# Optimization experiments

Measured on AMD Instinct MI355X. Metric: run time of the kernel, lower is better.

The kernel has to match this reference:

```python
import jax, jax.numpy as jnp
import numpy as np

B, N_PER, F = 8, 4096, 64
RATIO, RADIUS, K = 0.25, 0.2, 64
S = int(N_PER * RATIO)  # 1024 samples per cloud
NEG = -1e30


def setup_inputs() -> dict:
    key = jax.random.key(0)
    ks = jax.random.split(key, 8)
    pos = jax.random.uniform(ks[0], (B * N_PER, 3), dtype=jnp.float32)
    x = jax.random.normal(ks[1], (B * N_PER, F), dtype=jnp.float32)
    batch = jnp.repeat(jnp.arange(B, dtype=jnp.int32), N_PER)
    W1 = jax.random.normal(ks[2], (F + 3, 128), dtype=jnp.float32) * 0.05
    b1 = jnp.zeros((128,), jnp.float32)
    W2 = jax.random.normal(ks[3], (128, 128), dtype=jnp.float32) * 0.05
    b2 = jnp.zeros((128,), jnp.float32)
    W3 = jax.random.normal(ks[4], (128, 256), dtype=jnp.float32) * 0.05
    b3 = jnp.zeros((256,), jnp.float32)
    return {"x": x, "pos": pos, "batch": batch,
            "W1": W1, "b1": b1, "W2": W2, "b2": b2, "W3": W3, "b3": b3}


def _fps_single(p):
    """Farthest point sampling on one cloud p:[N,3] -> S int32 indices (seed idx 0)."""
    d0 = jnp.sum((p - p[0]) ** 2, axis=-1)  # [N]

    def step(min_d, _):
        nxt = jnp.argmax(min_d).astype(jnp.int32)
        d = jnp.sum((p - p[nxt]) ** 2, axis=-1)
        return jnp.minimum(min_d, d), nxt

    _, rest = jax.lax.scan(step, d0, None, length=S - 1)
    return jnp.concatenate([jnp.zeros((1,), jnp.int32), rest])


def reference(x, pos, batch, W1, b1, W2, b2, W3, b3):
    pos_b = pos.reshape(B, N_PER, 3)
    x_b = x.reshape(B, N_PER, F)
    batch_b = batch.reshape(B, N_PER)

    # --- FPS sampling (sequential scan, vmapped over clouds) ---
    idx = jax.vmap(_fps_single)(pos_b)                                  # [B,S]
    pos_s = jnp.take_along_axis(pos_b, idx[..., None], axis=1)          # [B,S,3]

    # --- radius neighbor search: nearest K within RADIUS (deterministic) ---
    d2 = jnp.sum((pos_s[:, :, None, :] - pos_b[:, None, :, :]) ** 2, -1)  # [B,S,N]
    neg = jnp.where(d2 <= RADIUS ** 2, -d2, NEG)
    vals, nbr = jax.lax.top_k(neg, K)                                   # [B,S,K]
    valid = vals > NEG / 2                                              # [B,S,K]

    # --- gather neighbor features / positions ---
    x_j = jnp.take_along_axis(x_b[:, None], nbr[..., None], axis=2)     # [B,S,K,F]
    pos_j = jnp.take_along_axis(pos_b[:, None], nbr[..., None], axis=2) # [B,S,K,3]
    rel = pos_j - pos_s[:, :, None, :]                                  # [B,S,K,3]

    # --- edge MLP (Lin+ReLU per PyG PointNetConv local_nn) ---
    h = jnp.concatenate([x_j, rel], axis=-1)                            # [B,S,K,F+3]
    h = jax.nn.relu(h @ W1 + b1)
    h = jax.nn.relu(h @ W2 + b2)
    h = jax.nn.relu(h @ W3 + b3)                                        # [B,S,K,256]

    # --- scatter-max aggregation over neighbors ---
    h = jnp.where(valid[..., None], h, NEG)
    out = jnp.max(h, axis=2)                                            # [B,S,256]
    out = jnp.where(out > NEG / 2, out, 0.0)

    x1 = out.reshape(B * S, -1)
    pos1 = pos_s.reshape(B * S, 3)
    batch1 = jnp.take_along_axis(batch_b, idx, axis=1).reshape(-1)
    return x1, pos1, batch1
```

## Files before the change

### kernel.cpp

```cpp
#include <hip/hip_runtime.h>
#include <hip/hip_bf16.h>
#include <stdint.h>

#define NPER 4096
#define NCLOUD 8
#define FD 64
#define SS 1024
#define NBK 64
#define CAP 512

typedef unsigned int u32;
typedef unsigned long long u64;
typedef __attribute__((ext_vector_type(8))) short short8v;
typedef __attribute__((ext_vector_type(8))) unsigned short ushort8v;
typedef __attribute__((ext_vector_type(4))) float f32x4;

__device__ __forceinline__ float fadd(float a, float b){ return __fadd_rn(a,b); }
__device__ __forceinline__ float fsub(float a, float b){ return __fsub_rn(a,b); }
__device__ __forceinline__ float fmul(float a, float b){ return __fmul_rn(a,b); }
__device__ __forceinline__ float dist2(float ax,float ay,float az,float bx,float by,float bz){
  float dx=fsub(ax,bx), dy=fsub(ay,by), dz=fsub(az,bz);
  return fadd(fadd(fmul(dx,dx),fmul(dy,dy)),fmul(dz,dz));
}
__device__ __forceinline__ unsigned short f2b(float v){
  __hip_bfloat16 h = __float2bfloat16(v);
  return *reinterpret_cast<unsigned short*>(&h);
}

template<int CTRL, int RMASK>
__device__ __forceinline__ float dppmaxf(float v){
  int t = __builtin_amdgcn_update_dpp(0, __float_as_int(v), CTRL, RMASK, 0xf, false);
  return fmaxf(v, __int_as_float(t));
}
template<int CTRL, int RMASK>
__device__ __forceinline__ void kmin_stage(u32& hi, u32& lo){
  u32 hio = (u32)__builtin_amdgcn_update_dpp(-1, (int)hi, CTRL, RMASK, 0xf, false);
  u32 loo = (u32)__builtin_amdgcn_update_dpp(-1, (int)lo, CTRL, RMASK, 0xf, false);
  u64 ko = ((u64)hio<<32)|loo, k = ((u64)hi<<32)|lo;
  bool g = ko < k;
  hi = g?hio:hi; lo = g?loo:lo;
}

#define LOADG(q, j0, j1, j2, j3) { \
    const float4* pv = (const float4*)(pb + (size_t)(base + q*4)*3); \
    float4 v0=pv[0], v1=pv[1], v2=pv[2]; \
    x##j0=v0.x; y##j0=v0.y; z##j0=v0.z; \
    x##j1=v0.w; y##j1=v1.x; z##j1=v1.y; \
    x##j2=v1.z; y##j2=v1.w; z##j2=v2.x; \
    x##j3=v2.y; y##j3=v2.z; z##j3=v2.w; \
    float4 c0; c0.x=x##j0; c0.y=y##j0; c0.z=z##j0; c0.w=0.f; spt[base+q*4+0]=c0; \
    float4 c1; c1.x=x##j1; c1.y=y##j1; c1.z=z##j1; c1.w=0.f; spt[base+q*4+1]=c1; \
    float4 c2; c2.x=x##j2; c2.y=y##j2; c2.z=z##j2; c2.w=0.f; spt[base+q*4+2]=c2; \
    float4 c3; c3.x=x##j3; c3.y=y##j3; c3.z=z##j3; c3.w=0.f; spt[base+q*4+3]=c3; \
  }
#define DINIT(j) m##j = dist2(x##j,y##j,z##j,p0x,p0y,p0z);
#define DUPD(j)  { float d = dist2(x##j,y##j,z##j,pnx,pny,pnz); m##j = fminf(m##j,d); }
#define ARGMAX16() { \
      bool c; float w0,w1,w2,w3,w4,w5,w6,w7; int i0,i1,i2,i3,i4,i5,i6,i7; \
      c=m1>m0;   w0=c?m1:m0;   i0=base+(c?1:0); \
      c=m3>m2;   w1=c?m3:m2;   i1=base+(c?3:2); \
      c=m5>m4;   w2=c?m5:m4;   i2=base+(c?5:4); \
      c=m7>m6;   w3=c?m7:m6;   i3=base+(c?7:6); \
      c=m9>m8;   w4=c?m9:m8;   i4=base+(c?9:8); \
      c=m11>m10; w5=c?m11:m10; i5=base+(c?11:10); \
      c=m13>m12; w6=c?m13:m12; i6=base+(c?13:12); \
      c=m15>m14; w7=c?m15:m14; i7=base+(c?15:14); \
      c=w1>w0; w0=c?w1:w0; i0=c?i1:i0; \
      c=w3>w2; w2=c?w3:w2; i2=c?i3:i2; \
      c=w5>w4; w4=c?w5:w4; i4=c?i5:i4; \
      c=w7>w6; w6=c?w7:w6; i6=c?i7:i6; \
      c=w2>w0; w0=c?w2:w0; i0=c?i2:i0; \
      c=w6>w4; w4=c?w6:w4; i4=c?i6:i4; \
      c=w4>w0; bv=c?w4:w0; bidx=c?i4:i0; \
    }
#define FPS_ITER(IT, WX, WY, WZ) { \
    float rv = bv; \
    rv = dppmaxf<0x121,0xf>(rv); \
    rv = dppmaxf<0x122,0xf>(rv); \
    rv = dppmaxf<0x124,0xf>(rv); \
    rv = dppmaxf<0x128,0xf>(rv); \
    rv = dppmaxf<0x142,0xa>(rv); \
    rv = dppmaxf<0x143,0xc>(rv); \
    const float wv = __int_as_float(__builtin_amdgcn_readlane(__float_as_int(rv), 63)); \
    u64 em = __ballot(bv == wv); \
    const int wl = __ffsll(em) - 1; \
    const int par = (IT) & 1; \
    if (lane == wl) \
      skey[par][w] = ((u64)__float_as_uint(wv)<<32) | (u64)(u32)(4095 - bidx); \
    __syncthreads(); \
    const u64* kp = &skey[par][0]; \
    u64 k0=kp[0], k1=kp[1], k2=kp[2], k3=kp[3]; \
    u64 ka = k0>k1?k0:k1, kb2 = k2>k3?k2:k3; \
    u64 km = ka>kb2?ka:kb2; \
    const int nxt = 4095 - (int)(km & 0xFFFull); \
    const float4 c = spt[nxt]; \
    const float pnx = __int_as_float(__builtin_amdgcn_readfirstlane(__float_as_int(c.x))); \
    const float pny = __int_as_float(__builtin_amdgcn_readfirstlane(__float_as_int(c.y))); \
    const float pnz = __int_as_float(__builtin_amdgcn_readfirstlane(__float_as_int(c.z))); \
    const bool mine = (t == ((IT) & 255)); \
    WX = mine ? pnx : WX; \
    WY = mine ? pny : WY; \
    WZ = mine ? pnz : WZ; \
    DUPD(0) DUPD(1) DUPD(2) DUPD(3) DUPD(4) DUPD(5) DUPD(6) DUPD(7) \
    DUPD(8) DUPD(9) DUPD(10) DUPD(11) DUPD(12) DUPD(13) DUPD(14) DUPD(15) \
    ARGMAX16() \
  }

__global__ __launch_bounds__(256, 1) void k_fps(const float* __restrict__ pos,
    float* __restrict__ pos_s, float* __restrict__ out_pos1, float* __restrict__ out_b1){
  __shared__ __align__(16) float4 spt[NPER];
  __shared__ __align__(16) u64 skey[2][4];
  const int b = blockIdx.x;
  const int t = threadIdx.x;
  const int w = t >> 6, lane = t & 63;
  const float* pb = pos + (size_t)b*NPER*3;
  const int base = t*16;
  float x0,x1,x2,x3,x4,x5,x6,x7,x8,x9,x10,x11,x12,x13,x14,x15;
  float y0,y1,y2,y3,y4,y5,y6,y7,y8,y9,y10,y11,y12,y13,y14,y15;
  float z0,z1,z2,z3,z4,z5,z6,z7,z8,z9,z10,z11,z12,z13,z14,z15;
  float m0,m1,m2,m3,m4,m5,m6,m7,m8,m9,m10,m11,m12,m13,m14,m15;
  LOADG(0, 0, 1, 2, 3)
  LOADG(1, 4, 5, 6, 7)
  LOADG(2, 8, 9, 10, 11)
  LOADG(3, 12, 13, 14, 15)
  const float p0x=pb[0], p0y=pb[1], p0z=pb[2];
  DINIT(0) DINIT(1) DINIT(2) DINIT(3) DINIT(4) DINIT(5) DINIT(6) DINIT(7)
  DINIT(8) DINIT(9) DINIT(10) DINIT(11) DINIT(12) DINIT(13) DINIT(14) DINIT(15)
  float bv; int bidx;
  ARGMAX16()
  float wx0=p0x, wy0=p0y, wz0=p0z;
  float wx1=0.f, wy1=0.f, wz1=0.f;
  float wx2=0.f, wy2=0.f, wz2=0.f;
  float wx3=0.f, wy3=0.f, wz3=0.f;
  for (int i=t;i<SS;i+=256) out_b1[b*SS+i] = (float)b;
  __syncthreads();
  for (int it=1;   it<256;  ++it) FPS_ITER(it, wx0, wy0, wz0)
  for (int it=256; it<512;  ++it) FPS_ITER(it, wx1, wy1, wz1)
  for (int it=512; it<768;  ++it) FPS_ITER(it, wx2, wy2, wz2)
  for (int it=768; it<1024; ++it) FPS_ITER(it, wx3, wy3, wz3)
  {
    const size_t g = (size_t)b*SS;
    size_t o = (g + t)*3;
    pos_s[o]=wx0; pos_s[o+1]=wy0; pos_s[o+2]=wz0;
    out_pos1[o]=wx0; out_pos1[o+1]=wy0; out_pos1[o+2]=wz0;
    o = (g + 256 + t)*3;
    pos_s[o]=wx1; pos_s[o+1]=wy1; pos_s[o+2]=wz1;
    out_pos1[o]=wx1; out_pos1[o+1]=wy1; out_pos1[o+2]=wz1;
    o = (g + 512 + t)*3;
    pos_s[o]=wx2; pos_s[o+1]=wy2; pos_s[o+2]=wz2;
    out_pos1[o]=wx2; out_pos1[o+1]=wy2; out_pos1[o+2]=wz2;
    o = (g + 768 + t)*3;
    pos_s[o]=wx3; pos_s[o+1]=wy3; pos_s[o+2]=wz3;
    out_pos1[o]=wx3; out_pos1[o+1]=wy3; out_pos1[o+2]=wz3;
  }
}

__device__ __forceinline__ u64 wave_min_u64(u64 k){
  u32 hi = (u32)(k>>32), lo = (u32)k;
  kmin_stage<0x121,0xf>(hi,lo);
  kmin_stage<0x122,0xf>(hi,lo);
  kmin_stage<0x124,0xf>(hi,lo);
  kmin_stage<0x128,0xf>(hi,lo);
  kmin_stage<0x142,0xa>(hi,lo);
  kmin_stage<0x143,0xc>(hi,lo);
  u32 rhi = (u32)__builtin_amdgcn_readlane((int)hi, 63);
  u32 rlo = (u32)__builtin_amdgcn_readlane((int)lo, 63);
  return ((u64)rhi<<32) | rlo;
}

__global__ __launch_bounds__(512) void k_nbr(const float* __restrict__ pos,
    const float* __restrict__ pos_s, unsigned short* __restrict__ nbr,
    const float* __restrict__ W1, const float* __restrict__ W2, const float* __restrict__ W3,
    unsigned short* __restrict__ Wt1, unsigned short* __restrict__ Wt2,
    unsigned short* __restrict__ Wt3){
  if (blockIdx.x >= 1024){
    int tt = (int)(blockIdx.x - 1024)*512 + (int)threadIdx.x;
    if (tt < 16384){
      int n = tt>>7, k = tt&127;
      Wt1[tt] = f2b(k < 67 ? W1[k*128+n] : 0.f);
    } else if (tt < 32768){
      int q = tt - 16384; int n = q>>7, k = q&127;
      Wt2[q] = f2b(W2[k*128+n]);
    } else {
      int q = tt - 32768; int n = q>>7, k = q&127;
      Wt3[q] = f2b(W3[k*256+n]);
    }
    return;
  }
  __shared__ float sxx[NPER], syy[NPER], szz[NPER];
  __shared__ u64 lst[8][CAP];
  __shared__ int cnt[8];
  const int t = threadIdx.x;
  const int w = t>>6, lane = t&63;
  const int gid0 = blockIdx.x*8;
  const int b = gid0 >> 10;
  const float* pb = pos + (size_t)b*NPER*3;
  for (int i=t;i<NPER;i+=512){
    sxx[i]=pb[i*3+0]; syy[i]=pb[i*3+1]; szz[i]=pb[i*3+2];
  }
  if (t<8) cnt[t]=0;
  __syncthreads();
  const int gid = gid0 + w;
  const float qx=pos_s[(size_t)gid*3+0], qy=pos_s[(size_t)gid*3+1], qz=pos_s[(size_t)gid*3+2];
  for (int i0=0;i0<NPER;i0+=64){
    int p = i0 + lane;
    float d = dist2(qx,qy,qz,sxx[p],syy[p],szz[p]);
    bool in = (d <= 0.04f);
    u64 m = __ballot(in);
    if (m){
      int tot = __popcll(m);
      int bse = 0;
      if (lane==0) bse = atomicAdd(&cnt[w], tot);
      bse = __shfl(bse, 0, 64);
      if (in){
        int o = bse + __popcll(m & ((1ull<<lane)-1ull));
        if (o < CAP) lst[w][o] = ((u64)__float_as_uint(d)<<12) | (u64)(u32)p;
      }
    }
  }
  int n = cnt[w];
  if (n > CAP) n = CAP;
  unsigned short outv = 0xFFFFu;
  if (n <= 64){
    if (lane < n) outv = (unsigned short)(lst[w][lane] & 0xFFFull);
  } else if (n <= 256){
    u64 c0=~0ull, c1=~0ull, c2=~0ull, c3=~0ull;
    c0 = lst[w][lane];
    if (lane+64  < n) c1 = lst[w][lane+64];
    if (lane+128 < n) c2 = lst[w][lane+128];
    if (lane+192 < n) c3 = lst[w][lane+192];
    for (int r=0;r<64;++r){
      u64 a  = c0<c1?c0:c1; int ia = c0<c1?0:1;
      u64 b2 = c2<c3?c2:c3; int ib = c2<c3?2:3;
      u64 bk = a<b2?a:b2;   int bp = a<b2?ia:ib;
      u64 rk = wave_min_u64(bk);
      if (bk == rk){
        if (bp==0) c0=~0ull; else if (bp==1) c1=~0ull;
        else if (bp==2) c2=~0ull; else c3=~0ull;
      }
      if (lane == r) outv = (unsigned short)(rk & 0xFFFull);
    }
  } else {
    for (int r=0;r<64;++r){
      u64 bk = ~0ull; int bp = -1;
      for (int i=lane;i<n;i+=64){
        u64 v = lst[w][i];
        bool lt = v < bk;
        bk = lt ? v : bk;
        bp = lt ? i : bp;
      }
      u64 rk = bk;
      #pragma unroll
      for (int off=32; off>=1; off>>=1){
        u64 o = __shfl_xor(rk, off, 64);
        rk = (o < rk) ? o : rk;
      }
      if (bk == rk) lst[w][bp] = ~0ull;
      if (lane == r) outv = (unsigned short)(rk & 0xFFFull);
    }
  }
  nbr[(size_t)gid*NBK + lane] = outv;
}

__device__ __forceinline__ void load_w512(const unsigned short* __restrict__ src,
    unsigned short* __restrict__ wb, int t){
  const int n = t>>2, q = t&3;
  const char* srow = (const char*)(src + n*128 + q*32);
  char* drow = (char*)wb + n*256;
  const u32 sw = (u32)(n&7)<<4;
  #pragma unroll
  for (int c=0;c<4;c++){
    ushort8v v = *(const ushort8v*)(srow + c*16);
    u32 colbyte = (u32)q*64 + (u32)c*16;
    *(ushort8v*)(drow + (colbyte ^ sw)) = v;
  }
}

__device__ __forceinline__ void load_w3full(const unsigned short* __restrict__ src,
    unsigned short* __restrict__ wb, int t){
  const int n = t>>1, hf = t&1;
  const char* srow = (const char*)(src + n*128 + hf*64);
  char* drow = (char*)wb + n*256;
  const u32 sw = (u32)(n&7)<<4;
  #pragma unroll
  for (int c=0;c<8;c++){
    ushort8v v = *(const ushort8v*)(srow + c*16);
    u32 colbyte = (u32)hf*128 + (u32)c*16;
    *(ushort8v*)(drow + (colbyte ^ sw)) = v;
  }
}

__device__ __forceinline__ void zero_acc(f32x4 acc[4][4]){
  #pragma unroll
  for (int i=0;i<4;i++){
    #pragma unroll
    for (int j=0;j<4;j++){
      f32x4 z = {0.f,0.f,0.f,0.f};
      acc[i][j] = z;
    }
  }
}

__device__ __forceinline__ void gemm_wave(const unsigned short* __restrict__ wb,
    const unsigned short* __restrict__ hb, int rbase, int nh, int lane, int ksteps,
    f32x4 acc[4][4]){
  const int li = lane & 15;
  const int lg = lane >> 4;
  for (int kk=0; kk<ksteps; ++kk){
    const u32 colb = (u32)(kk*64 + lg*16);
    short8v af[4], bfv[4];
    #pragma unroll
    for (int mt=0;mt<4;mt++){
      int wr = rbase + nh*64 + mt*16 + li;
      af[mt] = *(const short8v*)((const char*)wb + wr*256 + (colb ^ ((u32)(wr&7)<<4)));
    }
    #pragma unroll
    for (int nt=0;nt<4;nt++){
      int er = nt*16 + li;
      bfv[nt] = *(const short8v*)((const char*)hb + er*256 + (colb ^ ((u32)(er&7)<<4)));
    }
    #pragma unroll
    for (int mt=0;mt<4;mt++){
      #pragma unroll
      for (int nt=0;nt<4;nt++){
        acc[mt][nt] = __builtin_amdgcn_mfma_f32_16x16x32_bf16(af[mt], bfv[nt], acc[mt][nt], 0, 0, 0);
      }
    }
  }
}

__device__ __forceinline__ void epi_store(f32x4 acc[4][4], const float* __restrict__ bias,
    unsigned short* __restrict__ hb, int nh, int lane){
  const int li = lane & 15;
  const int lg = lane >> 4;
  #pragma unroll
  for (int mt=0;mt<4;mt++){
    const int c0 = nh*64 + mt*16 + lg*4;
    const float4 bb = *(const float4*)(bias + c0);
    #pragma unroll
    for (int nt=0;nt<4;nt++){
      const int r = nt*16 + li;
      f32x4 a = acc[mt][nt];
      float v0 = fmaxf(a.x + bb.x, 0.f);
      float v1 = fmaxf(a.y + bb.y, 0.f);
      float v2 = fmaxf(a.z + bb.z, 0.f);
      float v3 = fmaxf(a.w + bb.w, 0.f);
      u64 pk = (u64)f2b(v0) | ((u64)f2b(v1)<<16) | ((u64)f2b(v2)<<32) | ((u64)f2b(v3)<<48);
      u32 colbyte = (u32)(c0*2);
      *(u64*)((char*)hb + r*256 + (colbyte ^ ((u32)(r&7)<<4))) = pk;
    }
  }
}

__device__ __forceinline__ void epi_out(f32x4 acc[4][4], const float* __restrict__ b3g,
    float* __restrict__ outx, u64 vmask, int pass, int nh, int lane, int gs){
  const int li = lane & 15;
  const int lg = lane >> 4;
  #pragma unroll
  for (int mt=0;mt<4;mt++){
    const int c0 = pass*128 + nh*64 + mt*16 + lg*4;
    const float4 bb = *(const float4*)(b3g + c0);
    float vals[4];
    #pragma unroll
    for (int i=0;i<4;i++){
      float v = -1e30f;
      #pragma unroll
      for (int nt=0;nt<4;nt++){
        const int r = nt*16 + li;
        const bool ok = (vmask >> r) & 1ull;
        const float a = acc[mt][nt][i];
        v = fmaxf(v, ok ? a : -1e30f);
      }
      #pragma unroll
      for (int off=1; off<16; off<<=1){
        v = fmaxf(v, __shfl_xor(v, off, 64));
      }
      float biasv = (i==0)?bb.x:((i==1)?bb.y:((i==2)?bb.z:bb.w));
      vals[i] = fmaxf(v + biasv, 0.f);
    }
    if (li==0){
      float4 o; o.x=vals[0]; o.y=vals[1]; o.z=vals[2]; o.w=vals[3];
      *(float4*)(outx + (size_t)gs*256 + c0) = o;
    }
  }
}

__global__ __launch_bounds__(512) void k_mlp(const float* __restrict__ xg,
    const float* __restrict__ pg, const float* __restrict__ pos_s,
    const unsigned short* __restrict__ nbrg,
    const unsigned short* __restrict__ Wt1, const unsigned short* __restrict__ Wt2,
    const unsigned short* __restrict__ Wt3,
    const float* __restrict__ b1g, const float* __restrict__ b2g,
    const float* __restrict__ b3g, float* __restrict__ outx){
  __shared__ __align__(16) unsigned short hbuf[4][64][128];
  __shared__ __align__(16) unsigned short wbuf[256*128];
  __shared__ float spos[4][4];
  __shared__ unsigned short snbr[4][64];
  __shared__ u64 svalid[4];
  const int t = threadIdx.x;
  const int s0 = blockIdx.x*4;
  const int b = s0 >> 10;
  {
    u64* p = (u64*)hbuf;
    #pragma unroll
    for (int i=0;i<16;i++) p[t + i*512] = 0ull;
  }
  if (t < 4){
    spos[t][0]=pos_s[(size_t)(s0+t)*3+0];
    spos[t][1]=pos_s[(size_t)(s0+t)*3+1];
    spos[t][2]=pos_s[(size_t)(s0+t)*3+2];
  }
  if (t < 256){
    const int s=t>>6, r=t&63;
    unsigned short nb = nbrg[(size_t)(s0+s)*NBK + r];
    snbr[s][r]=nb;
    u64 m = __ballot(nb != 0xFFFFu);
    if (r==0) svalid[s]=m;
  }
  __syncthreads();
  {
    const int s = t>>7, r=(t>>1)&63, hf=t&1;
    const unsigned short nb = snbr[s][r];
    char* drow = (char*)hbuf + (s*64+r)*256;
    const u32 sw = (u32)(r&7)<<4;
    if (nb != 0xFFFFu){
      const float4* xr = (const float4*)(xg + ((size_t)b*NPER + nb)*FD + hf*32);
      #pragma unroll
      for (int c=0;c<4;c++){
        float4 v0 = xr[2*c];
        float4 v1 = xr[2*c+1];
        ushort8v u;
        u[0]=f2b(v0.x); u[1]=f2b(v0.y); u[2]=f2b(v0.z); u[3]=f2b(v0.w);
        u[4]=f2b(v1.x); u[5]=f2b(v1.y); u[6]=f2b(v1.z); u[7]=f2b(v1.w);
        u32 colbyte = (u32)hf*64 + (u32)c*16;
        *(ushort8v*)(drow + (colbyte ^ sw)) = u;
      }
      if (hf){
        const size_t po = ((size_t)b*NPER + nb)*3;
        float rx = fsub(pg[po+0], spos[s][0]);
        float ry = fsub(pg[po+1], spos[s][1]);
        float rz = fsub(pg[po+2], spos[s][2]);
        u64 pk = (u64)f2b(rx) | ((u64)f2b(ry)<<16) | ((u64)f2b(rz)<<32);
        *(u64*)(drow + (128u ^ sw)) = pk;
      }
    }
  }
  load_w512(Wt1, wbuf, t);
  __syncthreads();
  const int w = t>>6, lane = t&63;
  const int s = w>>1, nh = w&1;
  unsigned short* hb = &hbuf[s][0][0];
  f32x4 acc[4][4];
  zero_acc(acc);
  gemm_wave(wbuf, hb, 0, nh, lane, 3, acc);
  __syncthreads();
  epi_store(acc, b1g, hb, nh, lane);
  load_w512(Wt2, wbuf, t);
  __syncthreads();
  zero_acc(acc);
  gemm_wave(wbuf, hb, 0, nh, lane, 4, acc);
  __syncthreads();
  epi_store(acc, b2g, hb, nh, lane);
  load_w3full(Wt3, wbuf, t);
  __syncthreads();
  const u64 vm = svalid[s];
  zero_acc(acc);
  gemm_wave(wbuf, hb, 0,   nh, lane, 4, acc);
  epi_out(acc, b3g, outx, vm, 0, nh, lane, s0+s);
  zero_acc(acc);
  gemm_wave(wbuf, hb, 128, nh, lane, 4, acc);
  epi_out(acc, b3g, outx, vm, 1, nh, lane, s0+s);
}

extern "C" void kernel_launch(void* const* d_in, const int* in_sizes, int n_in,
                              void* d_out, int out_size, void* d_ws, size_t ws_size,
                              hipStream_t stream) {
  (void)in_sizes; (void)n_in; (void)out_size; (void)ws_size;
  const float* xg = (const float*)d_in[0];
  const float* pg = (const float*)d_in[1];
  const float* W1 = (const float*)d_in[3];
  const float* b1 = (const float*)d_in[4];
  const float* W2 = (const float*)d_in[5];
  const float* b2 = (const float*)d_in[6];
  const float* W3 = (const float*)d_in[7];
  const float* b3 = (const float*)d_in[8];
  float* outx = (float*)d_out;
  float* outp = outx + (size_t)8192*256;
  float* outb = outp + (size_t)8192*3;
  char* ws = (char*)d_ws;
  float* pos_s = (float*)ws;
  unsigned short* nbr = (unsigned short*)(ws + 98304);
  unsigned short* Wt1 = (unsigned short*)(ws + 98304 + 1048576);
  unsigned short* Wt2 = Wt1 + 16384;
  unsigned short* Wt3 = Wt2 + 16384;
  hipLaunchKernelGGL(k_fps, dim3(NCLOUD), dim3(256), 0, stream, pg, pos_s, outp, outb);
  hipLaunchKernelGGL(k_nbr, dim3(1024 + 128), dim3(512), 0, stream,
                     pg, pos_s, nbr, W1, W2, W3, Wt1, Wt2, Wt3);
  hipLaunchKernelGGL(k_mlp, dim3(8192/4), dim3(512), 0, stream,
                     xg, pg, pos_s, nbr, Wt1, Wt2, Wt3, b1, b2, b3, outx);
}
```

Baseline: 899.5 us.

## Fuse radius neighbor search into MLP kernel and split weight conversion

Moves the ball-query/top-K neighbor selection into the MLP kernel. Each block handles 4 samples, with 8 waves scanning half the cloud each, and the selected neighbors stay in shared memory instead of passing through a global nbr buffer. While 4 waves do the selection, the other 4 load W1 into shared memory. Weight bf16 conversion moves into its own small kernel launched before FPS. The trade-off is that each block now reloads the full cloud positions (48KB into reused shared memory), 2048 blocks instead of 1024, and only half the waves work during the top-K phase.

Measured after the change: 955.8 us. 1.06x slower.

```diff
diff --git a/kernel.cpp b/kernel.cpp
--- a/kernel.cpp
+++ b/kernel.cpp
@@ -155,6 +155,23 @@
   }
 }
 
+__global__ __launch_bounds__(256) void k_wconv(const float* __restrict__ W1,
+    const float* __restrict__ W2, const float* __restrict__ W3,
+    unsigned short* __restrict__ Wt1, unsigned short* __restrict__ Wt2,
+    unsigned short* __restrict__ Wt3){
+  int t = blockIdx.x*256 + threadIdx.x;
+  if (t < 16384){
+    int n = t>>7, k = t&127;
+    Wt1[t] = f2b(k < 67 ? W1[k*128+n] : 0.f);
+  } else if (t < 32768){
+    int q = t - 16384; int n = q>>7, k = q&127;
+    Wt2[q] = f2b(W2[k*128+n]);
+  } else if (t < 65536){
+    int q = t - 32768; int n = q>>7, k = q&127;
+    Wt3[q] = f2b(W3[k*256+n]);
+  }
+}
+
 __device__ __forceinline__ u64 wave_min_u64(u64 k){
   u32 hi = (u32)(k>>32), lo = (u32)k;
   kmin_stage<0x121,0xf>(hi,lo);
@@ -168,98 +185,18 @@
   return ((u64)rhi<<32) | rlo;
 }
 
-__global__ __launch_bounds__(512) void k_nbr(const float* __restrict__ pos,
-    const float* __restrict__ pos_s, unsigned short* __restrict__ nbr,
-    const float* __restrict__ W1, const float* __restrict__ W2, const float* __restrict__ W3,
-    unsigned short* __restrict__ Wt1, unsigned short* __restrict__ Wt2,
-    unsigned short* __restrict__ Wt3){
-  if (blockIdx.x >= 1024){
-    int tt = (int)(blockIdx.x - 1024)*512 + (int)threadIdx.x;
-    if (tt < 16384){
-      int n = tt>>7, k = tt&127;
-      Wt1[tt] = f2b(k < 67 ? W1[k*128+n] : 0.f);
-    } else if (tt < 32768){
-      int q = tt - 16384; int n = q>>7, k = q&127;
-      Wt2[q] = f2b(W2[k*128+n]);
-    } else {
-      int q = tt - 32768; int n = q>>7, k = q&127;
-      Wt3[q] = f2b(W3[k*256+n]);
-    }
-    return;
-  }
-  __shared__ float sxx[NPER], syy[NPER], szz[NPER];
-  __shared__ u64 lst[8][CAP];
-  __shared__ int cnt[8];
-  const int t = threadIdx.x;
-  const int w = t>>6, lane = t&63;
-  const int gid0 = blockIdx.x*8;
-  const int b = gid0 >> 10;
-  const float* pb = pos + (size_t)b*NPER*3;
-  for (int i=t;i<NPER;i+=512){
-    sxx[i]=pb[i*3+0]; syy[i]=pb[i*3+1]; szz[i]=pb[i*3+2];
-  }
-  if (t<8) cnt[t]=0;
-  __syncthreads();
-  const int gid = gid0 + w;
-  const float qx=pos_s[(size_t)gid*3+0], qy=pos_s[(size_t)gid*3+1], qz=pos_s[(size_t)gid*3+2];
-  for (int i0=0;i0<NPER;i0+=64){
-    int p = i0 + lane;
-    float d = dist2(qx,qy,qz,sxx[p],syy[p],szz[p]);
-    bool in = (d <= 0.04f);
-    u64 m = __ballot(in);
-    if (m){
-      int tot = __popcll(m);
-      int bse = 0;
-      if (lane==0) bse = atomicAdd(&cnt[w], tot);
-      bse = __shfl(bse, 0, 64);
-      if (in){
-        int o = bse + __popcll(m & ((1ull<<lane)-1ull));
-        if (o < CAP) lst[w][o] = ((u64)__float_as_uint(d)<<12) | (u64)(u32)p;
-      }
-    }
-  }
-  int n = cnt[w];
-  if (n > CAP) n = CAP;
-  unsigned short outv = 0xFFFFu;
-  if (n <= 64){
-    if (lane < n) outv = (unsigned short)(lst[w][lane] & 0xFFFull);
-  } else if (n <= 256){
-    u64 c0=~0ull, c1=~0ull, c2=~0ull, c3=~0ull;
-    c0 = lst[w][lane];
-    if (lane+64  < n) c1 = lst[w][lane+64];
-    if (lane+128 < n) c2 = lst[w][lane+128];
-    if (lane+192 < n) c3 = lst[w][lane+192];
-    for (int r=0;r<64;++r){
-      u64 a  = c0<c1?c0:c1; int ia = c0<c1?0:1;
-      u64 b2 = c2<c3?c2:c3; int ib = c2<c3?2:3;
-      u64 bk = a<b2?a:b2;   int bp = a<b2?ia:ib;
-      u64 rk = wave_min_u64(bk);
-      if (bk == rk){
-        if (bp==0) c0=~0ull; else if (bp==1) c1=~0ull;
-        else if (bp==2) c2=~0ull; else c3=~0ull;
-      }
-      if (lane == r) outv = (unsigned short)(rk & 0xFFFull);
-    }
-  } else {
-    for (int r=0;r<64;++r){
-      u64 bk = ~0ull; int bp = -1;
-      for (int i=lane;i<n;i+=64){
-        u64 v = lst[w][i];
-        bool lt = v < bk;
-        bk = lt ? v : bk;
-        bp = lt ? i : bp;
-      }
-      u64 rk = bk;
-      #pragma unroll
-      for (int off=32; off>=1; off>>=1){
-        u64 o = __shfl_xor(rk, off, 64);
-        rk = (o < rk) ? o : rk;
-      }
-      if (bk == rk) lst[w][bp] = ~0ull;
-      if (lane == r) outv = (unsigned short)(rk & 0xFFFull);
-    }
-  }
-  nbr[(size_t)gid*NBK + lane] = outv;
+__device__ __forceinline__ void load_w256(const unsigned short* __restrict__ src,
+    unsigned short* __restrict__ wb, int tt){
+  const int n = tt>>1, hf = tt&1;
+  const char* srow = (const char*)(src + n*128 + hf*64);
+  char* drow = (char*)wb + n*256;
+  const u32 sw = (u32)(n&7)<<4;
+  #pragma unroll
+  for (int c=0;c<8;c++){
+    ushort8v v = *(const ushort8v*)(srow + c*16);
+    u32 colbyte = (u32)hf*128 + (u32)c*16;
+    *(ushort8v*)(drow + (colbyte ^ sw)) = v;
+  }
 }
 
 __device__ __forceinline__ void load_w512(const unsigned short* __restrict__ src,
@@ -385,42 +322,117 @@
   }
 }
 
-__global__ __launch_bounds__(512) void k_mlp(const float* __restrict__ xg,
+__global__ __launch_bounds__(512) void k_fused(const float* __restrict__ xg,
     const float* __restrict__ pg, const float* __restrict__ pos_s,
-    const unsigned short* __restrict__ nbrg,
     const unsigned short* __restrict__ Wt1, const unsigned short* __restrict__ Wt2,
     const unsigned short* __restrict__ Wt3,
     const float* __restrict__ b1g, const float* __restrict__ b2g,
     const float* __restrict__ b3g, float* __restrict__ outx){
-  __shared__ __align__(16) unsigned short hbuf[4][64][128];
-  __shared__ __align__(16) unsigned short wbuf[256*128];
+  __shared__ __align__(16) unsigned char smem[131072];
   __shared__ float spos[4][4];
-  __shared__ unsigned short snbr[4][64];
+  __shared__ unsigned short snbr_l[4][64];
   __shared__ u64 svalid[4];
+  __shared__ int cnt[4];
+  float* sxx = (float*)smem;
+  float* syy = sxx + NPER;
+  float* szz = syy + NPER;
+  u64*   lst = (u64*)(smem + 49152);
+  unsigned short* hbuf = (unsigned short*)smem;
+  unsigned short* wbuf = (unsigned short*)(smem + 65536);
   const int t = threadIdx.x;
+  const int w = t>>6, lane = t&63;
   const int s0 = blockIdx.x*4;
   const int b = s0 >> 10;
   {
+    const float* pb = pg + (size_t)b*NPER*3;
+    for (int i=t;i<NPER;i+=512){
+      sxx[i]=pb[i*3+0]; syy[i]=pb[i*3+1]; szz[i]=pb[i*3+2];
+    }
+    if (t<4){
+      cnt[t]=0;
+      spos[t][0]=pos_s[(size_t)(s0+t)*3+0];
+      spos[t][1]=pos_s[(size_t)(s0+t)*3+1];
+      spos[t][2]=pos_s[(size_t)(s0+t)*3+2];
+    }
+    __syncthreads();
+    const int s = w & 3, half = w >> 2;
+    const int gid = s0 + s;
+    const float qx=pos_s[(size_t)gid*3+0], qy=pos_s[(size_t)gid*3+1], qz=pos_s[(size_t)gid*3+2];
+    u64* ls = lst + (size_t)s*CAP;
+    const int p0 = half*2048;
+    for (int i0=p0;i0<p0+2048;i0+=64){
+      int p = i0 + lane;
+      float d = dist2(qx,qy,qz,sxx[p],syy[p],szz[p]);
+      bool in = (d <= 0.04f);
+      u64 m = __ballot(in);
+      if (m){
+        int tot = __popcll(m);
+        int bse = 0;
+        if (lane==0) bse = atomicAdd(&cnt[s], tot);
+        bse = __shfl(bse, 0, 64);
+        if (in){
+          int o = bse + __popcll(m & ((1ull<<lane)-1ull));
+          if (o < CAP) ls[o] = ((u64)__float_as_uint(d)<<12) | (u64)(u32)p;
+        }
+      }
+    }
+    __syncthreads();
+    if (w < 4){
+      const int s2 = w;
+      u64* l2 = lst + (size_t)s2*CAP;
+      int n = cnt[s2];
+      if (n > CAP) n = CAP;
+      unsigned short outv = 0xFFFFu;
+      if (n <= 64){
+        if (lane < n) outv = (unsigned short)(l2[lane] & 0xFFFull);
+      } else if (n <= 256){
+        u64 c0=~0ull, c1=~0ull, c2=~0ull, c3=~0ull;
+        c0 = l2[lane];
+        if (lane+64  < n) c1 = l2[lane+64];
+        if (lane+128 < n) c2 = l2[lane+128];
+        if (lane+192 < n) c3 = l2[lane+192];
+        for (int r=0;r<64;++r){
+          u64 a  = c0<c1?c0:c1; int ia = c0<c1?0:1;
+          u64 b2 = c2<c3?c2:c3; int ib = c2<c3?2:3;
+          u64 bk = a<b2?a:b2;   int bp = a<b2?ia:ib;
+          u64 rk = wave_min_u64(bk);
+          if (bk == rk){
+            if (bp==0) c0=~0ull; else if (bp==1) c1=~0ull;
+            else if (bp==2) c2=~0ull; else c3=~0ull;
+          }
+          if (lane == r) outv = (unsigned short)(rk & 0xFFFull);
+        }
+      } else {
+        for (int r=0;r<64;++r){
+          u64 bk = ~0ull; int bp = -1;
+          for (int i=lane;i<n;i+=64){
+            u64 v = l2[i];
+            bool lt = v < bk;
+            bk = lt ? v : bk;
+            bp = lt ? i : bp;
+          }
+          u64 rk = wave_min_u64(bk);
+          if (bk == rk) l2[bp] = ~0ull;
+          if (lane == r) outv = (unsigned short)(rk & 0xFFFull);
+        }
+      }
+      snbr_l[s2][lane] = outv;
+      u64 vm = __ballot(outv != 0xFFFFu);
+      if (lane==0) svalid[s2] = vm;
+    } else {
+      load_w256(Wt1, wbuf, t - 256);
+    }
+    __syncthreads();
+  }
+  {
     u64* p = (u64*)hbuf;
     #pragma unroll
     for (int i=0;i<16;i++) p[t + i*512] = 0ull;
-  }
-  if (t < 4){
-    spos[t][0]=pos_s[(size_t)(s0+t)*3+0];
-    spos[t][1]=pos_s[(size_t)(s0+t)*3+1];
-    spos[t][2]=pos_s[(size_t)(s0+t)*3+2];
-  }
-  if (t < 256){
-    const int s=t>>6, r=t&63;
-    unsigned short nb = nbrg[(size_t)(s0+s)*NBK + r];
-    snbr[s][r]=nb;
-    u64 m = __ballot(nb != 0xFFFFu);
-    if (r==0) svalid[s]=m;
   }
   __syncthreads();
   {
     const int s = t>>7, r=(t>>1)&63, hf=t&1;
-    const unsigned short nb = snbr[s][r];
+    const unsigned short nb = snbr_l[s][r];
     char* drow = (char*)hbuf + (s*64+r)*256;
     const u32 sw = (u32)(r&7)<<4;
     if (nb != 0xFFFFu){
@@ -445,11 +457,9 @@
       }
     }
   }
-  load_w512(Wt1, wbuf, t);
-  __syncthreads();
-  const int w = t>>6, lane = t&63;
+  __syncthreads();
   const int s = w>>1, nh = w&1;
-  unsigned short* hb = &hbuf[s][0][0];
+  unsigned short* hb = hbuf + (size_t)s*64*128;
   f32x4 acc[4][4];
   zero_acc(acc);
   gemm_wave(wbuf, hb, 0, nh, lane, 3, acc);
@@ -489,13 +499,11 @@
   float* outb = outp + (size_t)8192*3;
   char* ws = (char*)d_ws;
   float* pos_s = (float*)ws;
-  unsigned short* nbr = (unsigned short*)(ws + 98304);
   unsigned short* Wt1 = (unsigned short*)(ws + 98304 + 1048576);
   unsigned short* Wt2 = Wt1 + 16384;
   unsigned short* Wt3 = Wt2 + 16384;
+  hipLaunchKernelGGL(k_wconv, dim3(256), dim3(256), 0, stream, W1, W2, W3, Wt1, Wt2, Wt3);
   hipLaunchKernelGGL(k_fps, dim3(NCLOUD), dim3(256), 0, stream, pg, pos_s, outp, outb);
-  hipLaunchKernelGGL(k_nbr, dim3(1024 + 128), dim3(512), 0, stream,
-                     pg, pos_s, nbr, W1, W2, W3, Wt1, Wt2, Wt3);
-  hipLaunchKernelGGL(k_mlp, dim3(8192/4), dim3(512), 0, stream,
-                     xg, pg, pos_s, nbr, Wt1, Wt2, Wt3, b1, b2, b3, outx);
-}
+  hipLaunchKernelGGL(k_fused, dim3(8192/4), dim3(512), 0, stream,
+                     xg, pg, pos_s, Wt1, Wt2, Wt3, b1, b2, b3, outx);
+}
```
